# Kernel tuning notes

Hardware: AMD Instinct MI355X
Metric: run time of the kernel (lower is better)

The kernel has to match this reference:

```python
import jax, jax.numpy as jnp
import numpy as np

# SS2D (VMamba) dims
B, H, W, C = 2, 48, 48, 96
D_INNER, D_STATE, DT_RANK, K = 192, 32, 6, 4


def _silu(x):
    return x * jax.nn.sigmoid(x)


def setup_inputs() -> dict:
    key = jax.random.key(0)
    ks = jax.random.split(key, 8)
    inputs = jax.random.normal(ks[0], (B, H, W, C), jnp.float32)
    in_proj_w = jax.random.normal(ks[1], (2 * D_INNER, C), jnp.float32) * 0.02
    conv_w = jax.random.normal(ks[2], (D_INNER, 1, 3, 3), jnp.float32) * 0.1
    conv_b = jnp.zeros((D_INNER,), jnp.float32)
    x_proj_w = jax.random.normal(ks[3], (K, DT_RANK + 2 * D_STATE, D_INNER), jnp.float32) * 0.02
    dt_projs_w = jax.random.normal(ks[4], (K, D_INNER, DT_RANK), jnp.float32) * 0.1
    dt_projs_b = jax.random.uniform(ks[5], (K, D_INNER), jnp.float32, -4.0, -2.0)
    # S4D-real init: A_log[n] = log(n+1), tiled over K*d_inner
    A_logs = jnp.log(jnp.tile(jnp.arange(1, D_STATE + 1, dtype=jnp.float32), (K * D_INNER, 1)))
    Ds = jnp.ones((K * D_INNER,), jnp.float32)
    ln_w = jnp.ones((D_INNER,), jnp.float32)
    ln_b = jnp.zeros((D_INNER,), jnp.float32)
    out_proj_w = jax.random.normal(ks[6], (C, D_INNER), jnp.float32) * 0.02
    return dict(inputs=inputs, in_proj_w=in_proj_w, conv_w=conv_w, conv_b=conv_b,
                x_proj_w=x_proj_w, dt_projs_w=dt_projs_w, dt_projs_b=dt_projs_b,
                A_logs=A_logs, Ds=Ds, ln_w=ln_w, ln_b=ln_b, out_proj_w=out_proj_w)


def _selective_scan(us, deltas, A, Bs, Cs, Ds_kd):
    # us, deltas: (B,K,d,L); Bs, Cs: (B,K,N,L); A: (K,d,N); Ds_kd: (K,d)
    u_l = jnp.moveaxis(us, -1, 0)      # (L,B,K,d)
    d_l = jnp.moveaxis(deltas, -1, 0)  # (L,B,K,d)
    B_l = jnp.moveaxis(Bs, -1, 0)      # (L,B,K,N)
    C_l = jnp.moveaxis(Cs, -1, 0)      # (L,B,K,N)
    h0 = jnp.zeros(us.shape[:3] + (A.shape[-1],), us.dtype)  # (B,K,d,N)

    def step(h, inp):
        u, d, b, c = inp
        dA = jnp.exp(d[..., None] * A)                    # (B,K,d,N)
        h = h * dA + (d * u)[..., None] * b[:, :, None, :]
        y = jnp.einsum('bkdn,bkn->bkd', h, c)
        return h, y

    _, ys = jax.lax.scan(step, h0, (u_l, d_l, B_l, C_l))
    ys = jnp.moveaxis(ys, 0, -1)  # (B,K,d,L)
    return ys + Ds_kd[None, :, :, None] * us


def _ss2d(x, in_proj_w, conv_w, conv_b, x_proj_w, dt_projs_w, dt_projs_b,
          A_logs, Ds, ln_w, ln_b, out_proj_w):
    b, h, w, c = x.shape
    L = h * w
    xz = jnp.einsum('bhwc,ec->bhwe', x, in_proj_w)          # (B,H,W,2*d_inner)
    x_, z = jnp.split(xz, 2, axis=-1)
    # depthwise 3x3 conv (NCHW), SAME padding
    x_ = jnp.transpose(x_, (0, 3, 1, 2))                    # (B,d,H,W)
    x_ = jax.lax.conv_general_dilated(x_, conv_w, (1, 1), 'SAME',
                                      feature_group_count=D_INNER,
                                      dimension_numbers=('NCHW', 'OIHW', 'NCHW'))
    x_ = _silu(x_ + conv_b[None, :, None, None])
    # 4-direction scan inputs
    x_hw = x_.reshape(b, D_INNER, L)
    x_wh = jnp.transpose(x_, (0, 1, 3, 2)).reshape(b, D_INNER, L)
    xs = jnp.stack([x_hw, x_wh], axis=1)                    # (B,2,d,L)
    xs = jnp.concatenate([xs, jnp.flip(xs, axis=-1)], axis=1)  # (B,4,d,L)
    x_dbl = jnp.einsum('bkdl,kcd->bkcl', xs, x_proj_w)      # (B,4,dt_rank+2N,L)
    dts = x_dbl[:, :, :DT_RANK]
    Bs = x_dbl[:, :, DT_RANK:DT_RANK + D_STATE]
    Cs = x_dbl[:, :, DT_RANK + D_STATE:]
    dts = jnp.einsum('bkrl,kdr->bkdl', dts, dt_projs_w)
    deltas = jax.nn.softplus(dts + dt_projs_b[None, :, :, None])
    A = -jnp.exp(A_logs).reshape(K, D_INNER, D_STATE)
    Ds_kd = Ds.reshape(K, D_INNER)
    out_y = _selective_scan(xs, deltas, A, Bs, Cs, Ds_kd)   # (B,4,d,L)
    inv_y = jnp.flip(out_y[:, 2:4], axis=-1)                # (B,2,d,L)
    wh_y = jnp.transpose(out_y[:, 1].reshape(b, D_INNER, w, h), (0, 1, 3, 2)).reshape(b, D_INNER, L)
    invwh_y = jnp.transpose(inv_y[:, 1].reshape(b, D_INNER, w, h), (0, 1, 3, 2)).reshape(b, D_INNER, L)
    y = out_y[:, 0] + inv_y[:, 0] + wh_y + invwh_y          # (B,d,L)
    y = jnp.transpose(y, (0, 2, 1)).reshape(b, h, w, D_INNER)
    # LayerNorm over channel dim
    mu = jnp.mean(y, axis=-1, keepdims=True)
    var = jnp.var(y, axis=-1, keepdims=True)
    y = (y - mu) * jax.lax.rsqrt(var + 1e-5) * ln_w + ln_b
    y = y * _silu(z)
    return jnp.einsum('bhwd,cd->bhwc', y, out_proj_w)


def reference(inputs, in_proj_w, conv_w, conv_b, x_proj_w, dt_projs_w, dt_projs_b,
              A_logs, Ds, ln_w, ln_b, out_proj_w):
    attn = _ss2d(inputs, in_proj_w, conv_w, conv_b, x_proj_w, dt_projs_w,
                 dt_projs_b, A_logs, Ds, ln_w, ln_b, out_proj_w)
    return inputs + attn
```

## Files before the change

### kernel.cpp

```cpp
#include <hip/hip_runtime.h>
#include <math.h>

#define B_ 2
#define H_ 48
#define W_ 48
#define C_ 96
#define D_ 192
#define L_ 2304
#define K_ 4
#define NS 32
#define RK 6
#define CD 70

#define NC 16
#define CL (L_/NC)
#define NCH (B_*K_*D_)

#define BDL (B_*D_*L_)
#define OFF_Z      0
#define OFF_XPRE   (OFF_Z    + BDL)
#define OFF_XHW    (OFF_XPRE + BDL)
#define OFF_XWH    (OFF_XHW  + BDL)
#define OFF_DELTA  (OFF_XWH  + BDL)
#define OFF_BS     (OFF_DELTA+ B_*K_*D_*L_)
#define OFF_CS     (OFF_BS   + B_*K_*L_*NS)
#define OFF_YS     (OFF_CS   + B_*K_*L_*NS)
#define OFF_YF     (OFF_YS   + B_*K_*L_*D_)

#define OFF_H0     OFF_YF

__global__ __launch_bounds__(256) void k1_inproj(const float* __restrict__ x,
        const float* __restrict__ w, float* __restrict__ ws) {
    __shared__ __align__(16) float Xs[24*128];
    int blk = blockIdx.x;
    int b = blk / 288;
    int rem = blk % 288;
    int l0 = (rem >> 2) * 32;
    int es = rem & 3;
    int tid = threadIdx.x;
    const float4* xs4 = (const float4*)(x + (size_t)(b*L_ + l0)*C_);
    #pragma unroll
    for (int it = 0; it < 3; ++it) {
        int i4 = it*256 + tid;
        float4 v = xs4[i4];
        int idx4 = i4*4;
        int p = idx4 / 96, c = idx4 % 96;
        *(float4*)&Xs[(c>>2)*128 + p*4] = v;
    }
    __syncthreads();
    int l = tid & 31, eg = tid >> 5;
    int pos = l0 + l;
    float acc[12];
    #pragma unroll
    for (int i = 0; i < 12; ++i) acc[i] = 0.f;
    const float4* wp[12];
    #pragma unroll
    for (int i = 0; i < 12; ++i) {
        int e = es*96 + eg*12 + i;
        wp[i] = (const float4*)(w + (size_t)e*96);
    }
    for (int q = 0; q < 24; ++q) {
        float4 xr = *(const float4*)&Xs[q*128 + l*4];
        #pragma unroll
        for (int i = 0; i < 12; ++i) {
            float4 wv = wp[i][q];
            acc[i] += xr.x*wv.x + xr.y*wv.y + xr.z*wv.z + xr.w*wv.w;
        }
    }
    if (es < 2) {
        float* xpre = ws + OFF_XPRE;
        #pragma unroll
        for (int i = 0; i < 12; ++i) {
            int e = es*96 + eg*12 + i;
            xpre[(size_t)(b*D_ + e)*L_ + pos] = acc[i];
        }
    } else {
        float* zp = ws + OFF_Z + (size_t)(b*L_ + pos)*D_ + (es-2)*96 + eg*12;
        #pragma unroll
        for (int q = 0; q < 3; ++q)
            *(float4*)&zp[q*4] = make_float4(acc[q*4], acc[q*4+1], acc[q*4+2], acc[q*4+3]);
    }
}

__global__ __launch_bounds__(256) void k2_conv(const float* __restrict__ cw,
        const float* __restrict__ cb, float* __restrict__ ws) {
    __shared__ float img[26*48];
    __shared__ float res[24*49];
    int blk = blockIdx.x;
    int bd = blk >> 1;
    int half = blk & 1;
    int d = bd % D_;
    int hh0 = half * 24;
    int tid = threadIdx.x;
    const float* xp = ws + OFF_XPRE + (size_t)bd*L_;
    for (int it = 0; it < 5; ++it) {
        int idx = it*256 + tid;
        if (idx < 26*48) {
            int gr = hh0 - 1 + idx/48;
            img[idx] = (gr >= 0 && gr < H_) ? xp[gr*48 + idx%48] : 0.f;
        }
    }
    float wr[9];
    #pragma unroll
    for (int j = 0; j < 9; ++j) wr[j] = cw[d*9 + j];
    float bias = cb[d];
    __syncthreads();
    float* hw = ws + OFF_XHW + (size_t)bd*L_ + hh0*48;
    for (int it = 0; it < 5; ++it) {
        int idx = it*256 + tid;
        if (idx < 24*48) {
            int r = idx/48, w0 = idx%48;
            float acc = bias;
            #pragma unroll
            for (int kh = 0; kh < 3; ++kh) {
                #pragma unroll
                for (int kw = 0; kw < 3; ++kw) {
                    int iw = w0 + kw - 1;
                    if (iw >= 0 && iw < W_)
                        acc = fmaf(img[(r+kh)*48 + iw], wr[kh*3 + kw], acc);
                }
            }
            float v = acc / (1.f + __expf(-acc));
            hw[idx] = v;
            res[r*49 + w0] = v;
        }
    }
    __syncthreads();
    float* wh = ws + OFF_XWH + (size_t)bd*L_;
    for (int it = 0; it < 5; ++it) {
        int idx = it*256 + tid;
        if (idx < 24*48) {
            int w0 = idx/24, r = idx%24;
            wh[w0*48 + hh0 + r] = res[r*49 + w0];
        }
    }
}

__global__ __launch_bounds__(256) void k3_xproj(const float* __restrict__ xpw,
        const float* __restrict__ dtw, const float* __restrict__ dtb,
        float* __restrict__ ws) {
    __shared__ __align__(16) float Xs[48*64];
    __shared__ float xd[CD*17];
    int blk = blockIdx.x;
    int b = blk / 576;
    int rem = blk % 576;
    int k = rem / 144;
    int l0 = (rem % 144) * 16;
    int tid = threadIdx.x;
    const float* src = ws + ((k & 1) ? OFF_XWH : OFF_XHW);
    bool flip = (k >= 2);
    #pragma unroll
    for (int it = 0; it < 12; ++it) {
        int idx = it*256 + tid;
        int d = idx >> 4, l = idx & 15;
        int pos = flip ? (L_ - 1 - (l0 + l)) : (l0 + l);
        Xs[(d>>2)*64 + l*4 + (d&3)] = src[(size_t)(b*D_ + d)*L_ + pos];
    }
    __syncthreads();
    int l = tid & 15, cg = tid >> 4;
    {
        float acc[5] = {0.f, 0.f, 0.f, 0.f, 0.f};
        const float4* wp[5];
        #pragma unroll
        for (int i = 0; i < 5; ++i) {
            int c = cg + 16*i;
            if (c >= CD) c = 0;
            wp[i] = (const float4*)(xpw + ((size_t)k*CD + c)*D_);
        }
        for (int q = 0; q < 48; ++q) {
            float4 xr = *(const float4*)&Xs[q*64 + l*4];
            #pragma unroll
            for (int i = 0; i < 5; ++i) {
                float4 wv = wp[i][q];
                acc[i] += xr.x*wv.x + xr.y*wv.y + xr.z*wv.z + xr.w*wv.w;
            }
        }
        #pragma unroll
        for (int i = 0; i < 5; ++i) {
            int c = cg + 16*i;
            if (c < CD) xd[c*17 + l] = acc[i];
        }
    }
    __syncthreads();
    {
        float r[6];
        #pragma unroll
        for (int rr = 0; rr < 6; ++rr) r[rr] = xd[rr*17 + l];
        float* dout = ws + OFF_DELTA + (size_t)(b*K_ + k)*D_*L_;
        int dg = tid >> 4;
        for (int i = 0; i < 12; ++i) {
            int d = dg*12 + i;
            const float* wdt = dtw + ((size_t)k*D_ + d)*6;
            float acc = dtb[k*D_ + d];
            #pragma unroll
            for (int rr = 0; rr < 6; ++rr) acc = fmaf(r[rr], wdt[rr], acc);
            float sp = fmaxf(acc, 0.f) + log1pf(__expf(-fabsf(acc)));
            dout[(size_t)d*L_ + l0 + l] = sp;
        }
    }
    {
        float* Bsp = ws + OFF_BS + ((size_t)(b*K_ + k)*L_ + l0)*NS;
        float* Csp = ws + OFF_CS + ((size_t)(b*K_ + k)*L_ + l0)*NS;
        int n = tid & 31, lq = tid >> 5;
        #pragma unroll
        for (int j = 0; j < 2; ++j) {
            int ll = lq + 8*j;
            Bsp[(size_t)ll*NS + n] = xd[(RK + n)*17 + ll];
            Csp[(size_t)ll*NS + n] = xd[(RK + NS + n)*17 + ll];
        }
    }
}

__global__ __launch_bounds__(512) void k4a_local(const float* __restrict__ Alogs,
        float* __restrict__ ws) {
    __shared__ float Pl[2][NC][NS];
    __shared__ float Hl[2][NC][NS];
    int blk = blockIdx.x;
    int bk = blk / 96;
    int p = blk % 96;
    int b = bk >> 2, k = bk & 3;
    int c = threadIdx.x >> 5;
    int n = threadIdx.x & 31;
    int dA = 2*p;
    float aA = -__expf(Alogs[((size_t)k*D_ + dA)*NS + n]);
    float aB = -__expf(Alogs[((size_t)k*D_ + dA + 1)*NS + n]);
    const float* dpA = ws + OFF_DELTA + (size_t)(bk*D_ + dA)*L_ + c*CL;
    const float* dpB = dpA + L_;
    const float* uA = ws + ((k & 1) ? OFF_XWH : OFF_XHW) + (size_t)(b*D_ + dA)*L_;
    const float* uB = uA + L_;
    const float* Bsp = ws + OFF_BS + ((size_t)bk*L_ + c*CL)*NS;
    bool flip = (k >= 2);
    float hA = 0.f, hB = 0.f, PA = 1.f, PB = 1.f;
    #pragma unroll 4
    for (int l = 0; l < CL; ++l) {
        int gl = c*CL + l;
        int gu = flip ? (L_ - 1 - gl) : gl;
        float dlA = dpA[l], dlB = dpB[l];
        float uAv = uA[gu], uBv = uB[gu];
        float bn = Bsp[l*NS + n];
        float eA = __expf(dlA * aA);
        float eB = __expf(dlB * aB);
        hA = fmaf(hA, eA, dlA*uAv*bn);
        hB = fmaf(hB, eB, dlB*uBv*bn);
        PA *= eA;
        PB *= eB;
    }
    Pl[0][c][n] = PA; Pl[1][c][n] = PB;
    Hl[0][c][n] = hA; Hl[1][c][n] = hB;
    __syncthreads();
    if (threadIdx.x < 64) {
        int ch = threadIdx.x >> 5, nn = threadIdx.x & 31;
        float* H0p = ws + OFF_H0 + (size_t)(bk*D_ + dA + ch)*NC*NS + nn;
        float h = 0.f;
        #pragma unroll
        for (int cc = 0; cc < NC; ++cc) {
            H0p[cc*NS] = h;
            h = fmaf(h, Pl[ch][cc][nn], Hl[ch][cc][nn]);
        }
    }
}

__global__ __launch_bounds__(512) void k4c_scan(const float* __restrict__ Alogs,
        const float* __restrict__ Dsp, float* __restrict__ ws) {
    __shared__ float yld[CL*32];
    int blk = blockIdx.x;
    int dg = blk % 6;
    int c  = (blk / 6) % NC;
    int bk = blk / (6*NC);
    int b = bk >> 2, k = bk & 3;
    int sw = threadIdx.x >> 5;
    int n  = threadIdx.x & 31;
    int dA = dg*32 + sw;
    int dB = dA + 16;
    float aA = -__expf(Alogs[((size_t)k*D_ + dA)*NS + n]);
    float aB = -__expf(Alogs[((size_t)k*D_ + dB)*NS + n]);
    float dcA = Dsp[k*D_ + dA];
    float dcB = Dsp[k*D_ + dB];
    const float* dpA = ws + OFF_DELTA + (size_t)(bk*D_ + dA)*L_ + c*CL;
    const float* dpB = dpA + 16*L_;
    const float* uA = ws + ((k & 1) ? OFF_XWH : OFF_XHW) + (size_t)(b*D_ + dA)*L_;
    const float* uB = uA + 16*L_;
    const float* Bsp = ws + OFF_BS + ((size_t)bk*L_ + c*CL)*NS;
    const float* Csp = ws + OFF_CS + ((size_t)bk*L_ + c*CL)*NS;
    bool flip = (k >= 2);
    float hA = ws[OFF_H0 + (size_t)(bk*D_ + dA)*NC*NS + c*NS + n];
    float hB = ws[OFF_H0 + (size_t)(bk*D_ + dB)*NC*NS + c*NS + n];
    int g = n >> 3;
    int off = ((g & 1) << 1) | (g >> 1);
    for (int lb = 0; lb < CL; lb += 4) {
        float yA[4], yB[4], uuA[4], uuB[4];
        #pragma unroll
        for (int j = 0; j < 4; ++j) {
            int l = lb + j;
            int gl = c*CL + l;
            int gu = flip ? (L_ - 1 - gl) : gl;
            float dlA = dpA[l], dlB = dpB[l];
            float uAv = uA[gu], uBv = uB[gu];
            float bn = Bsp[l*NS + n];
            float cn = Csp[l*NS + n];
            hA = fmaf(hA, __expf(dlA*aA), dlA*uAv*bn);
            hB = fmaf(hB, __expf(dlB*aB), dlB*uBv*bn);
            yA[j] = hA * cn; yB[j] = hB * cn;
            uuA[j] = uAv;    uuB[j] = uBv;
        }
        #pragma unroll
        for (int j = 0; j < 4; ++j) {
            yA[j] += __shfl_xor(yA[j], 16);
            yB[j] += __shfl_xor(yB[j], 16);
        }
        float zA0 = (n & 16) ? yA[1] : yA[0];
        float zA1 = (n & 16) ? yA[3] : yA[2];
        float zB0 = (n & 16) ? yB[1] : yB[0];
        float zB1 = (n & 16) ? yB[3] : yB[2];
        zA0 += __shfl_xor(zA0, 8); zA1 += __shfl_xor(zA1, 8);
        zB0 += __shfl_xor(zB0, 8); zB1 += __shfl_xor(zB1, 8);
        float wA = (n & 8) ? zA1 : zA0;
        float wB = (n & 8) ? zB1 : zB0;
        wA += __shfl_xor(wA, 4); wA += __shfl_xor(wA, 2); wA += __shfl_xor(wA, 1);
        wB += __shfl_xor(wB, 4); wB += __shfl_xor(wB, 2); wB += __shfl_xor(wB, 1);
        float uaA = (n & 16) ? uuA[1] : uuA[0];
        float ubA = (n & 16) ? uuA[3] : uuA[2];
        float usA = (n & 8) ? ubA : uaA;
        float uaB = (n & 16) ? uuB[1] : uuB[0];
        float ubB = (n & 16) ? uuB[3] : uuB[2];
        float usB = (n & 8) ? ubB : uaB;
        if ((n & 7) == 0) {
            yld[(lb + off)*32 + sw]      = fmaf(dcA, usA, wA);
            yld[(lb + off)*32 + sw + 16] = fmaf(dcB, usB, wB);
        }
    }
    __syncthreads();
    float* ysp = ws + OFF_YS + ((size_t)bk*L_ + c*CL)*D_ + dg*32;
    #pragma unroll
    for (int it = 0; it < 9; ++it) {
        int idx = it*512 + threadIdx.x;
        int l = idx >> 5, dd = idx & 31;
        ysp[(size_t)l*D_ + dd] = yld[idx];
    }
}

__global__ __launch_bounds__(256) void k56_fused(const float* __restrict__ lnw,
        const float* __restrict__ lnb, const float* __restrict__ w,
        const float* __restrict__ xin, float* __restrict__ out,
        const float* __restrict__ ws) {
    __shared__ __align__(16) float Ys[48*64];
    __shared__ float redS[16][17];
    __shared__ float redQ[16][17];
    __shared__ float muS[16], rsS[16];
    __shared__ float outT[16*97];
    int blk = blockIdx.x;
    int b = blk / 144;
    int l0 = (blk % 144) * 16;
    int tid = threadIdx.x;
    int hh = l0 / W_;
    int w0b = l0 % W_;
    const float* ys = ws + OFF_YS + (size_t)b*K_*L_*D_;
    #pragma unroll
    for (int it = 0; it < 3; ++it) {
        int i4 = it*256 + tid;
        int p = i4 / 48, c48 = i4 % 48;
        int pos = l0 + p;
        int poswh = (w0b + p)*H_ + hh;
        const float4* y0 = (const float4*)(ys + (size_t)(0*L_ + pos)*D_);
        const float4* y2 = (const float4*)(ys + (size_t)(2*L_ + (L_-1-pos))*D_);
        const float4* y1 = (const float4*)(ys + (size_t)(1*L_ + poswh)*D_);
        const float4* y3 = (const float4*)(ys + (size_t)(3*L_ + (L_-1-poswh))*D_);
        float4 a = y0[c48], bb = y2[c48], cc = y1[c48], dd = y3[c48];
        float4 v = make_float4(a.x+bb.x+cc.x+dd.x, a.y+bb.y+cc.y+dd.y,
                               a.z+bb.z+cc.z+dd.z, a.w+bb.w+cc.w+dd.w);
        *(float4*)&Ys[c48*64 + p*4] = v;
    }
    __syncthreads();
    {
        int p = tid & 15, g = tid >> 4;
        float s = 0.f, q = 0.f;
        #pragma unroll
        for (int j = 0; j < 3; ++j) {
            int qq = g*3 + j;
            #pragma unroll
            for (int sx = 0; sx < 4; ++sx) {
                float v = Ys[qq*64 + p*4 + sx];
                s += v; q += v*v;
            }
        }
        redS[p][g] = s; redQ[p][g] = q;
    }
    __syncthreads();
    if (tid < 16) {
        float s = 0.f, q = 0.f;
        #pragma unroll
        for (int g = 0; g < 16; ++g) { s += redS[tid][g]; q += redQ[tid][g]; }
        float mu  = s * (1.f/192.f);
        float var = q * (1.f/192.f) - mu*mu;
        muS[tid] = mu;
        rsS[tid] = rsqrtf(var + 1e-5f);
    }
    __syncthreads();
    #pragma unroll
    for (int it = 0; it < 3; ++it) {
        int i4 = it*256 + tid;
        int p = i4 / 48, c48 = i4 % 48;
        int pos = l0 + p;
        float4 v  = *(float4*)&Ys[c48*64 + p*4];
        float4 wv = *(const float4*)(lnw + c48*4);
        float4 bv = *(const float4*)(lnb + c48*4);
        float4 zv = *(const float4*)(ws + OFF_Z + (size_t)(b*L_ + pos)*D_ + c48*4);
        float mu = muS[p], rs = rsS[p];
        float o0 = ((v.x-mu)*rs*wv.x + bv.x) * (zv.x / (1.f + __expf(-zv.x)));
        float o1 = ((v.y-mu)*rs*wv.y + bv.y) * (zv.y / (1.f + __expf(-zv.y)));
        float o2 = ((v.z-mu)*rs*wv.z + bv.z) * (zv.z / (1.f + __expf(-zv.z)));
        float o3 = ((v.w-mu)*rs*wv.w + bv.w) * (zv.w / (1.f + __expf(-zv.w)));
        *(float4*)&Ys[c48*64 + p*4] = make_float4(o0, o1, o2, o3);
    }
    __syncthreads();
    int l = tid & 15, cg = tid >> 4;
    float acc[6];
    #pragma unroll
    for (int i = 0; i < 6; ++i) acc[i] = 0.f;
    const float4* wp[6];
    #pragma unroll
    for (int i = 0; i < 6; ++i) {
        int c = cg*6 + i;
        wp[i] = (const float4*)(w + (size_t)c*D_);
    }
    for (int q = 0; q < 48; ++q) {
        float4 xr = *(const float4*)&Ys[q*64 + l*4];
        #pragma unroll
        for (int i = 0; i < 6; ++i) {
            float4 wv = wp[i][q];
            acc[i] += xr.x*wv.x + xr.y*wv.y + xr.z*wv.z + xr.w*wv.w;
        }
    }
    #pragma unroll
    for (int i = 0; i < 6; ++i) outT[l*97 + cg*6 + i] = acc[i];
    __syncthreads();
    #pragma unroll
    for (int it = 0; it < 6; ++it) {
        int idx = it*256 + tid;
        int p = idx / 96, cc = idx % 96;
        size_t o = (size_t)(b*L_ + l0 + p)*C_ + cc;
        out[o] = xin[o] + outT[p*97 + cc];
    }
}

extern "C" void kernel_launch(void* const* d_in, const int* in_sizes, int n_in,
                              void* d_out, int out_size, void* d_ws, size_t ws_size,
                              hipStream_t stream) {
    const float* x        = (const float*)d_in[0];
    const float* in_proj  = (const float*)d_in[1];
    const float* conv_w   = (const float*)d_in[2];
    const float* conv_b   = (const float*)d_in[3];
    const float* x_proj_w = (const float*)d_in[4];
    const float* dt_w     = (const float*)d_in[5];
    const float* dt_b     = (const float*)d_in[6];
    const float* A_logs   = (const float*)d_in[7];
    const float* Ds       = (const float*)d_in[8];
    const float* ln_w     = (const float*)d_in[9];
    const float* ln_b     = (const float*)d_in[10];
    const float* out_w    = (const float*)d_in[11];
    float* out = (float*)d_out;
    float* ws  = (float*)d_ws;

    k1_inproj <<<576,  256, 0, stream>>>(x, in_proj, ws);
    k2_conv   <<<768,  256, 0, stream>>>(conv_w, conv_b, ws);
    k3_xproj  <<<1152, 256, 0, stream>>>(x_proj_w, dt_w, dt_b, ws);
    k4a_local <<<768,  512, 0, stream>>>(A_logs, ws);
    k4c_scan  <<<768,  512, 0, stream>>>(A_logs, Ds, ws);
    k56_fused <<<288,  256, 0, stream>>>(ln_w, ln_b, out_w, x, out, ws);
}
```

Measured before the change: 285.3 us.

## Precompute delta*u chunk-major, use exp2, move D skip to epilogue, chunk-local ys layout

The x-projection kernel now also writes delta*u into a chunk-contiguous buffer, so both scan kernels read a contiguous stream instead of gathering flipped or transposed u and multiplying per step. The scans use raw v_exp_f32 with log2e folded into A. The D*u skip term is moved out of the scan into the final fused kernel, which sums Ds over directions and adds it using the hw-ordered x. The scan writes ys in a block-contiguous layout that the epilogue indexes directly. The cost is an extra buffer write in k3 and more index arithmetic in the epilogue.

```diff
diff --git a/kernel.cpp b/kernel.cpp
--- a/kernel.cpp
+++ b/kernel.cpp
@@ -27,7 +27,13 @@
 #define OFF_YS     (OFF_CS   + B_*K_*L_*NS)
 #define OFF_YF     (OFF_YS   + B_*K_*L_*D_)
 
+#define OFF_DU     OFF_YS
+
 #define OFF_H0     OFF_YF
+
+__device__ __forceinline__ float fexp2(float x) {
+    float r; asm("v_exp_f32 %0, %1" : "=v"(r) : "v"(x)); return r;
+}
 
 __global__ __launch_bounds__(256) void k1_inproj(const float* __restrict__ x,
         const float* __restrict__ w, float* __restrict__ ws) {
@@ -186,7 +192,11 @@
         float r[6];
         #pragma unroll
         for (int rr = 0; rr < 6; ++rr) r[rr] = xd[rr*17 + l];
-        float* dout = ws + OFF_DELTA + (size_t)(b*K_ + k)*D_*L_;
+        int bk = b*K_ + k;
+        float* dout = ws + OFF_DELTA + (size_t)bk*D_*L_;
+        int cch = l0 / CL;
+        int lc  = l0 - cch*CL + l;
+        float* dup = ws + OFF_DU + ((size_t)(bk*NC + cch))*D_*CL;
         int dg = tid >> 4;
         for (int i = 0; i < 12; ++i) {
             int d = dg*12 + i;
@@ -196,6 +206,8 @@
             for (int rr = 0; rr < 6; ++rr) acc = fmaf(r[rr], wdt[rr], acc);
             float sp = fmaxf(acc, 0.f) + log1pf(__expf(-fabsf(acc)));
             dout[(size_t)d*L_ + l0 + l] = sp;
+            float uv = Xs[(d>>2)*64 + l*4 + (d&3)];
+            dup[(size_t)d*CL + lc] = sp * uv;
         }
     }
     {
@@ -218,30 +230,27 @@
     int blk = blockIdx.x;
     int bk = blk / 96;
     int p = blk % 96;
-    int b = bk >> 2, k = bk & 3;
+    int k = bk & 3;
     int c = threadIdx.x >> 5;
     int n = threadIdx.x & 31;
     int dA = 2*p;
-    float aA = -__expf(Alogs[((size_t)k*D_ + dA)*NS + n]);
-    float aB = -__expf(Alogs[((size_t)k*D_ + dA + 1)*NS + n]);
+    float aA2 = -__expf(Alogs[((size_t)k*D_ + dA)*NS + n]) * 1.44269504f;
+    float aB2 = -__expf(Alogs[((size_t)k*D_ + dA + 1)*NS + n]) * 1.44269504f;
     const float* dpA = ws + OFF_DELTA + (size_t)(bk*D_ + dA)*L_ + c*CL;
     const float* dpB = dpA + L_;
-    const float* uA = ws + ((k & 1) ? OFF_XWH : OFF_XHW) + (size_t)(b*D_ + dA)*L_;
-    const float* uB = uA + L_;
+    const float* duA = ws + OFF_DU + ((size_t)(bk*NC + c)*D_ + dA)*CL;
+    const float* duB = duA + CL;
     const float* Bsp = ws + OFF_BS + ((size_t)bk*L_ + c*CL)*NS;
-    bool flip = (k >= 2);
     float hA = 0.f, hB = 0.f, PA = 1.f, PB = 1.f;
     #pragma unroll 4
     for (int l = 0; l < CL; ++l) {
-        int gl = c*CL + l;
-        int gu = flip ? (L_ - 1 - gl) : gl;
         float dlA = dpA[l], dlB = dpB[l];
-        float uAv = uA[gu], uBv = uB[gu];
+        float duAv = duA[l], duBv = duB[l];
         float bn = Bsp[l*NS + n];
-        float eA = __expf(dlA * aA);
-        float eB = __expf(dlB * aB);
-        hA = fmaf(hA, eA, dlA*uAv*bn);
-        hB = fmaf(hB, eB, dlB*uBv*bn);
+        float eA = fexp2(dlA * aA2);
+        float eB = fexp2(dlB * aB2);
+        hA = fmaf(hA, eA, duAv*bn);
+        hB = fmaf(hB, eB, duBv*bn);
         PA *= eA;
         PB *= eB;
     }
@@ -261,47 +270,41 @@
 }
 
 __global__ __launch_bounds__(512) void k4c_scan(const float* __restrict__ Alogs,
-        const float* __restrict__ Dsp, float* __restrict__ ws) {
+        float* __restrict__ ws) {
     __shared__ float yld[CL*32];
     int blk = blockIdx.x;
     int dg = blk % 6;
     int c  = (blk / 6) % NC;
     int bk = blk / (6*NC);
-    int b = bk >> 2, k = bk & 3;
+    int k = bk & 3;
     int sw = threadIdx.x >> 5;
     int n  = threadIdx.x & 31;
     int dA = dg*32 + sw;
     int dB = dA + 16;
-    float aA = -__expf(Alogs[((size_t)k*D_ + dA)*NS + n]);
-    float aB = -__expf(Alogs[((size_t)k*D_ + dB)*NS + n]);
-    float dcA = Dsp[k*D_ + dA];
-    float dcB = Dsp[k*D_ + dB];
+    float aA2 = -__expf(Alogs[((size_t)k*D_ + dA)*NS + n]) * 1.44269504f;
+    float aB2 = -__expf(Alogs[((size_t)k*D_ + dB)*NS + n]) * 1.44269504f;
     const float* dpA = ws + OFF_DELTA + (size_t)(bk*D_ + dA)*L_ + c*CL;
     const float* dpB = dpA + 16*L_;
-    const float* uA = ws + ((k & 1) ? OFF_XWH : OFF_XHW) + (size_t)(b*D_ + dA)*L_;
-    const float* uB = uA + 16*L_;
+    const float* duA = ws + OFF_DU + ((size_t)(bk*NC + c)*D_ + dA)*CL;
+    const float* duB = duA + 16*CL;
     const float* Bsp = ws + OFF_BS + ((size_t)bk*L_ + c*CL)*NS;
     const float* Csp = ws + OFF_CS + ((size_t)bk*L_ + c*CL)*NS;
-    bool flip = (k >= 2);
     float hA = ws[OFF_H0 + (size_t)(bk*D_ + dA)*NC*NS + c*NS + n];
     float hB = ws[OFF_H0 + (size_t)(bk*D_ + dB)*NC*NS + c*NS + n];
     int g = n >> 3;
     int off = ((g & 1) << 1) | (g >> 1);
     for (int lb = 0; lb < CL; lb += 4) {
-        float yA[4], yB[4], uuA[4], uuB[4];
+        float yA[4], yB[4];
         #pragma unroll
         for (int j = 0; j < 4; ++j) {
             int l = lb + j;
-            int gl = c*CL + l;
-            int gu = flip ? (L_ - 1 - gl) : gl;
             float dlA = dpA[l], dlB = dpB[l];
-            float uAv = uA[gu], uBv = uB[gu];
+            float duAv = duA[l], duBv = duB[l];
             float bn = Bsp[l*NS + n];
             float cn = Csp[l*NS + n];
-            hA = fmaf(hA, __expf(dlA*aA), dlA*uAv*bn);
-            hB = fmaf(hB, __expf(dlB*aB), dlB*uBv*bn);
+            hA = fmaf(hA, fexp2(dlA*aA2), duAv*bn);
+            hB = fmaf(hB, fexp2(dlB*aB2), duBv*bn);
             yA[j] = hA * cn; yB[j] = hB * cn;
-            uuA[j] = uAv;    uuB[j] = uBv;
         }
         #pragma unroll
         for (int j = 0; j < 4; ++j) {
@@ -318,35 +321,29 @@
         float wB = (n & 8) ? zB1 : zB0;
         wA += __shfl_xor(wA, 4); wA += __shfl_xor(wA, 2); wA += __shfl_xor(wA, 1);
         wB += __shfl_xor(wB, 4); wB += __shfl_xor(wB, 2); wB += __shfl_xor(wB, 1);
-        float uaA = (n & 16) ? uuA[1] : uuA[0];
-        float ubA = (n & 16) ? uuA[3] : uuA[2];
-        float usA = (n & 8) ? ubA : uaA;
-        float uaB = (n & 16) ? uuB[1] : uuB[0];
-        float ubB = (n & 16) ? uuB[3] : uuB[2];
-        float usB = (n & 8) ? ubB : uaB;
         if ((n & 7) == 0) {
-            yld[(lb + off)*32 + sw]      = fmaf(dcA, usA, wA);
-            yld[(lb + off)*32 + sw + 16] = fmaf(dcB, usB, wB);
-        }
-    }
-    __syncthreads();
-    float* ysp = ws + OFF_YS + ((size_t)bk*L_ + c*CL)*D_ + dg*32;
+            yld[(lb + off)*32 + sw]      = wA;
+            yld[(lb + off)*32 + sw + 16] = wB;
+        }
+    }
+    __syncthreads();
+    float* ysp = ws + OFF_YS + (size_t)blk*(CL*32);
     #pragma unroll
     for (int it = 0; it < 9; ++it) {
         int idx = it*512 + threadIdx.x;
-        int l = idx >> 5, dd = idx & 31;
-        ysp[(size_t)l*D_ + dd] = yld[idx];
+        ysp[idx] = yld[idx];
     }
 }
 
 __global__ __launch_bounds__(256) void k56_fused(const float* __restrict__ lnw,
-        const float* __restrict__ lnb, const float* __restrict__ w,
-        const float* __restrict__ xin, float* __restrict__ out,
-        const float* __restrict__ ws) {
+        const float* __restrict__ lnb, const float* __restrict__ dsp,
+        const float* __restrict__ w, const float* __restrict__ xin,
+        float* __restrict__ out, const float* __restrict__ ws) {
     __shared__ __align__(16) float Ys[48*64];
     __shared__ float redS[16][17];
     __shared__ float redQ[16][17];
     __shared__ float muS[16], rsS[16];
+    __shared__ float Dsum[D_];
     __shared__ float outT[16*97];
     int blk = blockIdx.x;
     int b = blk / 144;
@@ -354,21 +351,35 @@
     int tid = threadIdx.x;
     int hh = l0 / W_;
     int w0b = l0 % W_;
-    const float* ys = ws + OFF_YS + (size_t)b*K_*L_*D_;
+    if (tid < D_) Dsum[tid] = dsp[tid] + dsp[D_+tid] + dsp[2*D_+tid] + dsp[3*D_+tid];
+    const float* ysb = ws + OFF_YS;
+    int bk0 = b*K_;
     #pragma unroll
     for (int it = 0; it < 3; ++it) {
         int i4 = it*256 + tid;
         int p = i4 / 48, c48 = i4 % 48;
-        int pos = l0 + p;
-        int poswh = (w0b + p)*H_ + hh;
-        const float4* y0 = (const float4*)(ys + (size_t)(0*L_ + pos)*D_);
-        const float4* y2 = (const float4*)(ys + (size_t)(2*L_ + (L_-1-pos))*D_);
-        const float4* y1 = (const float4*)(ys + (size_t)(1*L_ + poswh)*D_);
-        const float4* y3 = (const float4*)(ys + (size_t)(3*L_ + (L_-1-poswh))*D_);
-        float4 a = y0[c48], bb = y2[c48], cc = y1[c48], dd = y3[c48];
+        int pos    = l0 + p;
+        int posr   = L_ - 1 - pos;
+        int poswh  = (w0b + p)*H_ + hh;
+        int poswhr = L_ - 1 - poswh;
+        int dsub = c48 >> 3;
+        int doff = (c48 & 7) * 4;
+        float4 a  = *(const float4*)&ysb[((((size_t)(bk0+0)*NC + pos   /CL)*6 + dsub)*CL + pos   %CL)*32 + doff];
+        float4 bb = *(const float4*)&ysb[((((size_t)(bk0+2)*NC + posr  /CL)*6 + dsub)*CL + posr  %CL)*32 + doff];
+        float4 cc = *(const float4*)&ysb[((((size_t)(bk0+1)*NC + poswh /CL)*6 + dsub)*CL + poswh %CL)*32 + doff];
+        float4 dd = *(const float4*)&ysb[((((size_t)(bk0+3)*NC + poswhr/CL)*6 + dsub)*CL + poswhr%CL)*32 + doff];
         float4 v = make_float4(a.x+bb.x+cc.x+dd.x, a.y+bb.y+cc.y+dd.y,
                                a.z+bb.z+cc.z+dd.z, a.w+bb.w+cc.w+dd.w);
         *(float4*)&Ys[c48*64 + p*4] = v;
+    }
+    __syncthreads();
+    const float* xhw = ws + OFF_XHW;
+    #pragma unroll
+    for (int it = 0; it < 12; ++it) {
+        int idx = it*256 + tid;
+        int d = idx >> 4, p = idx & 15;
+        float xv = xhw[(size_t)(b*D_ + d)*L_ + l0 + p];
+        Ys[(d>>2)*64 + p*4 + (d&3)] += Dsum[d]*xv;
     }
     __syncthreads();
     {
@@ -465,6 +476,6 @@
     k2_conv   <<<768,  256, 0, stream>>>(conv_w, conv_b, ws);
     k3_xproj  <<<1152, 256, 0, stream>>>(x_proj_w, dt_w, dt_b, ws);
     k4a_local <<<768,  512, 0, stream>>>(A_logs, ws);
-    k4c_scan  <<<768,  512, 0, stream>>>(A_logs, Ds, ws);
-    k56_fused <<<288,  256, 0, stream>>>(ln_w, ln_b, out_w, x, out, ws);
-}
+    k4c_scan  <<<768,  512, 0, stream>>>(A_logs, ws);
+    k56_fused <<<288,  256, 0, stream>>>(ln_w, ln_b, Ds, out_w, x, out, ws);
+}
```

New measurement: 286.7 us. Within noise of the previous version (+0.5%).
